# Performance work log

Hardware: AMD Instinct MI355X
Metric: run time of the kernel (lower is better)

The kernel has to match this reference:

```python
import jax, jax.numpy as jnp
import numpy as np

B, N, D = 4, 256, 256
H, DH = 4, 64
INNER = H * DH
L, MULT, EDGE, KNN = 2, 2, 11, 3
LN_EPS = 1e-5


def _layernorm(x, w, b):
    m = x.mean(-1, keepdims=True)
    v = ((x - m) ** 2).mean(-1, keepdims=True)
    return (x - m) * jax.lax.rsqrt(v + LN_EPS) * w + b


def _gelu(x):
    return jax.nn.gelu(x, approximate=False)  # torch nn.GELU default = exact erf


def _knn_pair_mask(coords, valid, k):
    # coords [B,M,2], valid [B,M] -> symmetric KNN adjacency among neighbors
    Bm, M = valid.shape
    d = jnp.sqrt(jnp.sum((coords[:, :, None, :] - coords[:, None, :, :]) ** 2, -1))
    eye = jnp.eye(M, dtype=bool)[None]
    inv = ~(valid[:, :, None] & valid[:, None, :])
    d = jnp.where(inv | eye, jnp.inf, d)
    neg, idx = jax.lax.top_k(-d, k)  # k smallest distances
    finite = jnp.isfinite(neg)
    bi = jnp.arange(Bm)[:, None, None]
    ri = jnp.arange(M)[None, :, None]
    mask = jnp.zeros((Bm, M, M), bool).at[bi, ri, idx].set(finite)
    mask = mask | jnp.swapaxes(mask, 1, 2)
    return mask & ~eye


def _build_graph(x, coords):
    # valid node mask (infer_valid_node_mask) and hop ids (infer_hop_ids)
    valid = (jnp.abs(x).sum(-1) > 0).at[:, 0].set(True)
    hop = jnp.ones((B, N), jnp.int32).at[:, 0].set(0)
    hop = hop.at[:, 1 + (N - 1) // 2:].set(2)
    eye = jnp.eye(N, dtype=bool)[None]
    adj = jnp.broadcast_to(eye, (B, N, N))
    nv = valid[:, 1:]
    adj = adj.at[:, 0, 1:].set(nv)
    adj = adj.at[:, 1:, 0].set(nv)
    npm = _knn_pair_mask(coords[:, 1:], nv, min(KNN, N - 2))
    adj = adj.at[:, 1:, 1:].set(adj[:, 1:, 1:] | npm)
    vp = valid[:, :, None] & valid[:, None, :]
    adj = adj & (vp | eye)
    # edge features [B,N,N,11]
    rel = coords[:, None, :, :] - coords[:, :, None, :]  # coords[j]-coords[i]
    dx, dy = rel[..., 0], rel[..., 1]
    dist = jnp.sqrt(dx ** 2 + dy ** 2 + 1e-8)
    cdist = jnp.sqrt(coords[..., 0] ** 2 + coords[..., 1] ** 2 + 1e-8)
    nvm = valid.at[:, 0].set(False)
    cd = jnp.where(nvm, cdist, 0.0)
    cnt = jnp.clip(nvm.sum(-1), 1).astype(x.dtype)
    ls = cd.sum(-1) / cnt
    ls = jnp.where(ls > 0, ls, 1.0)
    ndist = dist / jnp.clip(ls, 1e-6)[:, None, None]
    idx = jnp.arange(N)
    ones2 = jnp.ones((N, N), bool)
    qic = (idx[:, None] == 0) & ones2
    kic = (idx[None, :] == 0) & ones2
    eye2 = jnp.eye(N, dtype=bool)
    isnn = ~(qic | kic | eye2)
    same_hop = hop[:, :, None] == hop[:, None, :]
    hop_delta = jnp.abs(hop[:, None, :] - hop[:, :, None]).astype(x.dtype)
    same_ct = jnp.zeros((B, N, N), x.dtype)  # cell_inf is None
    f = lambda m: jnp.broadcast_to(m.astype(x.dtype), (B, N, N))
    edge_attr = jnp.stack(
        [dx, dy, dist, ndist, f(qic), f(kic), f(eye2), f(isnn),
         same_hop.astype(x.dtype), hop_delta, same_ct], -1)
    return adj, edge_attr


def _forward(x, coords, Wq, Wk, Wv, eb_w1, eb_b1, eb_w2, eb_b2,
             ev_w1, ev_b1, ev_w2, ev_b2, Wo, bo,
             ln1_w, ln1_b, ln2_w, ln2_b, ff_w1, ff_b1, ff_w2, ff_b2):
    adj, e = _build_graph(x, coords)
    scale = DH ** -0.5
    big = jnp.finfo(x.dtype).max
    for l in range(L):
        xn = _layernorm(x, ln1_w[l], ln1_b[l])
        q = (xn @ Wq[l]).reshape(B, N, H, DH).transpose(0, 2, 1, 3)  # b h n d
        k = (xn @ Wk[l]).reshape(B, N, H, DH).transpose(0, 2, 1, 3)
        v = (xn @ Wv[l]).reshape(B, N, H, DH).transpose(0, 2, 1, 3)
        eb = _gelu(e @ eb_w1[l] + eb_b1[l]) @ eb_w2[l] + eb_b2[l]  # [B,N,N,H]
        ev = _gelu(e @ ev_w1[l] + ev_b1[l]) @ ev_w2[l] + ev_b2[l]  # [B,N,N,INNER]
        ev = ev.reshape(B, N, N, H, DH).transpose(0, 3, 1, 2, 4)   # b h i j d
        sim = jnp.einsum('bhid,bhjd->bhij', q, k) * scale + eb.transpose(0, 3, 1, 2)
        sim = jnp.where(adj[:, None], sim, -big)
        attn = jax.nn.softmax(sim, -1)
        msgs = v[:, :, None, :, :] + ev                            # value injection
        out = jnp.einsum('bhij,bhijd->bhid', attn, msgs)
        out = out.transpose(0, 2, 1, 3).reshape(B, N, INNER) @ Wo[l] + bo[l]
        x = x + out
        xn2 = _layernorm(x, ln2_w[l], ln2_b[l])
        hg = xn2 @ ff_w1[l] + ff_b1[l]
        a, g = jnp.split(hg, 2, -1)  # GEGLU
        x = x + ((a * _gelu(g)) @ ff_w2[l] + ff_b2[l])
    return x


def setup_inputs() -> dict:
    key = jax.random.key(0)
    ks = iter(jax.random.split(key, 32))
    w = lambda shape, s=0.05: jax.random.normal(next(ks), shape, jnp.float32) * s
    return {
        'x': jax.random.normal(next(ks), (B, N, D), jnp.float32),
        'coords': jax.random.normal(next(ks), (B, N, 2), jnp.float32) * 3.0,
        'Wq': w((L, D, INNER)), 'Wk': w((L, D, INNER)), 'Wv': w((L, D, INNER)),
        'eb_w1': w((L, EDGE, INNER)), 'eb_b1': jnp.zeros((L, INNER)),
        'eb_w2': w((L, INNER, H)), 'eb_b2': jnp.zeros((L, H)),
        'ev_w1': w((L, EDGE, INNER)), 'ev_b1': jnp.zeros((L, INNER)),
        'ev_w2': w((L, INNER, INNER)), 'ev_b2': jnp.zeros((L, INNER)),
        'Wo': w((L, INNER, D)), 'bo': jnp.zeros((L, D)),
        'ln1_w': jnp.ones((L, D)), 'ln1_b': jnp.zeros((L, D)),
        'ln2_w': jnp.ones((L, D)), 'ln2_b': jnp.zeros((L, D)),
        'ff_w1': w((L, D, 2 * MULT * D)), 'ff_b1': jnp.zeros((L, 2 * MULT * D)),
        'ff_w2': w((L, MULT * D, D)), 'ff_b2': jnp.zeros((L, D)),
    }


def reference(x, coords, Wq, Wk, Wv, eb_w1, eb_b1, eb_w2, eb_b2,
              ev_w1, ev_b1, ev_w2, ev_b2, Wo, bo,
              ln1_w, ln1_b, ln2_w, ln2_b, ff_w1, ff_b1, ff_w2, ff_b2):
    return _forward(x, coords, Wq, Wk, Wv, eb_w1, eb_b1, eb_w2, eb_b2,
                    ev_w1, ev_b1, ev_w2, ev_b2, Wo, bo,
                    ln1_w, ln1_b, ln2_w, ln2_b, ff_w1, ff_b1, ff_w2, ff_b2)
```

## Files before the change

### kernel.cpp

```cpp
#include <hip/hip_runtime.h>


#define MAXE  16384
#define NONX  22080
#define BF16_TOTAL 1441792

typedef __attribute__((ext_vector_type(8))) short bf16x8;
typedef __attribute__((ext_vector_type(4))) float f32x4;

struct PtrPack { const void* p[23]; };

__device__ __forceinline__ float bf2f(unsigned short s) {
  return __uint_as_float(((unsigned)s) << 16);
}
__device__ __forceinline__ unsigned short f2bf(float f) {
  unsigned u = __float_as_uint(f);
  u += 0x7fffu + ((u >> 16) & 1u);
  return (unsigned short)(u >> 16);
}
__device__ __forceinline__ float gelu_f(float x) {
  return 0.5f * x * (1.0f + erff(x * 0.70710678118654752440f));
}
__device__ __forceinline__ float wave_red_sum(float v) {
#pragma unroll
  for (int o = 32; o > 0; o >>= 1) v += __shfl_xor(v, o);
  return v;
}

__device__ __forceinline__ void edge_feats(int i, int j, float cxi, float cyi,
                                           float cxj, float cyj, float lsd, float* e) {
  float dx = cxj - cxi, dy = cyj - cyi;
  float dist = sqrtf(dx * dx + dy * dy + 1e-8f);
  e[0] = dx; e[1] = dy; e[2] = dist; e[3] = dist / lsd;
  bool qic = (i == 0), kic = (j == 0), eye = (i == j);
  e[4] = qic ? 1.f : 0.f;
  e[5] = kic ? 1.f : 0.f;
  e[6] = eye ? 1.f : 0.f;
  e[7] = (!qic && !kic && !eye) ? 1.f : 0.f;
  int hi = (i == 0) ? 0 : ((i < 128) ? 1 : 2);
  int hj = (j == 0) ? 0 : ((j < 128) ? 1 : 2);
  e[8] = (hi == hj) ? 1.f : 0.f;
  int hd = hj - hi;
  e[9] = (float)(hd < 0 ? -hd : hd);
}

__global__ __launch_bounds__(256) void k_convert(PtrPack pp, float* __restrict__ blobF,
                                                 unsigned short* __restrict__ blobB,
                                                 int* __restrict__ valid,
                                                 float* __restrict__ rowsum,
                                                 int* __restrict__ gctr) {
  bool isf32 = (*(const unsigned*)pp.p[15] == 0x3F800000u);
  int t = threadIdx.x;
  if (blockIdx.x == 0 && t == 0) *gctr = 0;
  if (blockIdx.x < 1024) {
    if (blockIdx.x < 32) rowsum[blockIdx.x * 256 + t] = 0.f;
    int r = blockIdx.x;
    int idx = r * 256 + t;
    float v = isf32 ? ((const float*)pp.p[0])[idx]
                    : bf2f(((const unsigned short*)pp.p[0])[idx]);
    blobF[idx] = v;
    __shared__ float s[4];
    float a = wave_red_sum(fabsf(v));
    if ((t & 63) == 0) s[t >> 6] = a;
    __syncthreads();
    if (t == 0) valid[r] = ((s[0] + s[1] + s[2] + s[3]) > 0.0f) || ((r & 255) == 0);
  } else {
    const int fst[16] = {0,2048,7680,8192,10240,10304,15936,16448,16960,17472,17984,18496,19008,19520,21568,22080};
    const int fsz[15] = {2048,5632,512,2048,8,5632,512,512,512,512,512,512,512,2048,512};
    const int fin[15] = {1,5,6,7,8,9,10,12,14,15,16,17,18,20,22};
    const int bst[8]  = {0,131072,262144,393216,524288,655360,1179648,1441792};
    const int bin[7]  = {2,3,4,13,11,19,21};
    for (int idx = (blockIdx.x - 1024) * 256 + t; idx < NONX + BF16_TOTAL; idx += 1024 * 256) {
      if (idx < NONX) {
        int s = 0;
        while (s < 14 && idx >= fst[s + 1]) ++s;
        int e = idx - fst[s];
        float v = 0.f;
        if (e < fsz[s]) v = isf32 ? ((const float*)pp.p[fin[s]])[e]
                                  : bf2f(((const unsigned short*)pp.p[fin[s]])[e]);
        blobF[262144 + idx] = v;
      } else {
        int bi = idx - NONX;
        int s = 0;
        while (s < 6 && bi >= bst[s + 1]) ++s;
        int e = bi - bst[s];
        blobB[bi] = isf32 ? f2bf(((const float*)pp.p[bin[s]])[e])
                          : ((const unsigned short*)pp.p[bin[s]])[e];
      }
    }
  }
}

__global__ __launch_bounds__(256) void k_knn(const float* __restrict__ cf,
                                             const int* __restrict__ valid,
                                             int* __restrict__ knn) {
  int blk = blockIdx.x;
  int b = blk >> 6;
  int w = threadIdx.x >> 6, lane = threadIdx.x & 63;
  int i = (blk & 63) * 4 + w;
  const float2* cc = (const float2*)(cf + b * 512);
  float2 ci = cc[i];
  bool vi = (valid[b * 256 + i] != 0) && (i != 0);
  unsigned long long key[4];
#pragma unroll
  for (int k = 0; k < 4; ++k) {
    int j = lane + 64 * k;
    bool ok = vi && (j != 0) && (j != i) && (valid[b * 256 + j] != 0);
    unsigned long long kk = ~0ull;
    if (ok) {
      float2 cj = cc[j];
      float dx = ci.x - cj.x, dy = ci.y - cj.y;
      float dd = sqrtf(dx * dx + dy * dy);
      kk = (((unsigned long long)__float_as_uint(dd)) << 32) | (unsigned)j;
    }
    key[k] = kk;
  }
  int out[3];
#pragma unroll
  for (int rnd = 0; rnd < 3; ++rnd) {
    unsigned long long m = key[0];
    if (key[1] < m) m = key[1];
    if (key[2] < m) m = key[2];
    if (key[3] < m) m = key[3];
#pragma unroll
    for (int o = 32; o > 0; o >>= 1) {
      unsigned long long om = __shfl_xor(m, o);
      if (om < m) m = om;
    }
    out[rnd] = (m != ~0ull) ? (int)(m & 0xFFFFFFFFull) : -1;
#pragma unroll
    for (int k = 0; k < 4; ++k)
      if (key[k] == m) key[k] = ~0ull;
  }
  if (lane == 0) {
    knn[(b * 256 + i) * 3 + 0] = out[0];
    knn[(b * 256 + i) * 3 + 1] = out[1];
    knn[(b * 256 + i) * 3 + 2] = out[2];
  }
}

__global__ __launch_bounds__(256) void k_csr(const float* __restrict__ cf,
                                             const int* __restrict__ valid,
                                             const int* __restrict__ knn,
                                             float* __restrict__ lsbuf,
                                             int* __restrict__ deg, int* __restrict__ rowptr,
                                             int* __restrict__ rowof, int* __restrict__ colsb,
                                             int* __restrict__ gctr) {
  int b = blockIdx.x, t = threadIdx.x;
  __shared__ unsigned adjw[256][8];
  __shared__ float sred[8];
  __shared__ int wsum[4];
  __shared__ int sbase;

  int r = b * 256 + t;
  float cx = cf[r * 2 + 0], cy = cf[r * 2 + 1];
  int lv = valid[r];
#pragma unroll
  for (int w = 0; w < 8; ++w) adjw[t][w] = 0u;
  __syncthreads();

  atomicOr(&adjw[t][t >> 5], 1u << (t & 31));
  if (t >= 1 && lv) {
    atomicOr(&adjw[0][t >> 5], 1u << (t & 31));
    atomicOr(&adjw[t][0], 1u);
  }
#pragma unroll
  for (int s = 0; s < 3; ++s) {
    int j = knn[r * 3 + s];
    if (j >= 0) {
      atomicOr(&adjw[t][j >> 5], 1u << (j & 31));
      atomicOr(&adjw[j][t >> 5], 1u << (t & 31));
    }
  }
  float cdist = sqrtf(cx * cx + cy * cy + 1e-8f);
  int nvm = (t >= 1) && lv;
  float rs = wave_red_sum(nvm ? cdist : 0.0f);
  float rc = wave_red_sum(nvm ? 1.0f : 0.0f);
  if ((t & 63) == 0) { sred[t >> 6] = rs; sred[4 + (t >> 6)] = rc; }
  __syncthreads();

  if (t == 0) {
    float totd = sred[0] + sred[1] + sred[2] + sred[3];
    float totc = sred[4] + sred[5] + sred[6] + sred[7];
    float ls = totd / fmaxf(totc, 1.0f);
    ls = (ls > 0.0f) ? ls : 1.0f;
    lsbuf[b] = fmaxf(ls, 1e-6f);
  }

  int dg = 0;
#pragma unroll
  for (int w = 0; w < 8; ++w) dg += __popc(adjw[t][w]);

  int lane = t & 63, wv = t >> 6;
  int x = dg;
#pragma unroll
  for (int off = 1; off < 64; off <<= 1) {
    int y = __shfl_up(x, off);
    if (lane >= off) x += y;
  }
  if (lane == 63) wsum[wv] = x;
  __syncthreads();
  if (t == 0) sbase = atomicAdd(gctr, wsum[0] + wsum[1] + wsum[2] + wsum[3]);
  __syncthreads();
  int woff = 0;
#pragma unroll
  for (int k2 = 0; k2 < 4; ++k2) woff += (k2 < wv) ? wsum[k2] : 0;
  int off0 = sbase + woff + x - dg;

  rowptr[r] = off0;
  deg[r] = dg;
  int o = off0;
#pragma unroll
  for (int w = 0; w < 8; ++w) {
    unsigned bits = adjw[t][w];
    while (bits) {
      int bp = __ffs(bits) - 1;
      colsb[o] = w * 32 + bp;
      rowof[o] = r;
      ++o;
      bits &= bits - 1;
    }
  }
}

template <int AMODE, int OMODE>
__device__ __forceinline__ void mfma_body(const void* Aptr, int lda,
                                          const unsigned short* __restrict__ B, int ldb, int n0B,
                                          const float* __restrict__ bias,
                                          const float* resid,
                                          void* C, int ldc, int n0C,
                                          int m0, int K, bool obf,
                                          const float* __restrict__ lnG,
                                          const float* __restrict__ lnB) {
  __shared__ short As[16][72];
  __shared__ short Bs[64][72];
  __shared__ float sG[256], sB2[256], sMean[16], sRstd[16];
  int t = threadIdx.x, lane = t & 63, w = t >> 6;

  if (AMODE == 3) {
    sG[t] = lnG[t]; sB2[t] = lnB[t];
    int row = t >> 4, sub = t & 15;
    const float* xr = (const float*)Aptr + (size_t)(m0 + row) * lda + sub * 16;
    float s = 0.f, ss = 0.f;
#pragma unroll
    for (int ii = 0; ii < 4; ++ii) {
      float4 v4 = *(const float4*)(xr + ii * 4);
      s += v4.x + v4.y + v4.z + v4.w;
      ss += v4.x * v4.x + v4.y * v4.y + v4.z * v4.z + v4.w * v4.w;
    }
    s += __shfl_xor(s, 1); s += __shfl_xor(s, 2);
    s += __shfl_xor(s, 4); s += __shfl_xor(s, 8);
    ss += __shfl_xor(ss, 1); ss += __shfl_xor(ss, 2);
    ss += __shfl_xor(ss, 4); ss += __shfl_xor(ss, 8);
    if (sub == 0) {
      float m = s * (1.f / 256.f);
      float var = ss * (1.f / 256.f) - m * m;
      sMean[row] = m;
      sRstd[row] = 1.f / sqrtf(var + 1e-5f);
    }
    __syncthreads();
  }

  f32x4 acc;
  acc[0] = 0.f; acc[1] = 0.f; acc[2] = 0.f; acc[3] = 0.f;

  int am = t >> 3, ak = (t & 7) * 8;
  int bk = t >> 2, bn = (t & 3) * 16;

  for (int k0 = 0; k0 < K; k0 += 64) {
    if (t < 128) {
      if (AMODE == 0) {
        const unsigned short* ap = (const unsigned short*)Aptr + (size_t)(m0 + am) * lda + k0 + ak;
        *(bf16x8*)&As[am][ak] = *(const bf16x8*)ap;
      } else if (AMODE == 1) {
        const float* ap = (const float*)Aptr + (size_t)(m0 + am) * lda + k0 + ak;
        float4 a0 = *(const float4*)ap;
        float4 a1 = *(const float4*)(ap + 4);
        float4 g0 = *(const float4*)(ap + 512);
        float4 g1 = *(const float4*)(ap + 516);
        short tmp[8];
        tmp[0] = (short)f2bf(a0.x * gelu_f(g0.x));
        tmp[1] = (short)f2bf(a0.y * gelu_f(g0.y));
        tmp[2] = (short)f2bf(a0.z * gelu_f(g0.z));
        tmp[3] = (short)f2bf(a0.w * gelu_f(g0.w));
        tmp[4] = (short)f2bf(a1.x * gelu_f(g1.x));
        tmp[5] = (short)f2bf(a1.y * gelu_f(g1.y));
        tmp[6] = (short)f2bf(a1.z * gelu_f(g1.z));
        tmp[7] = (short)f2bf(a1.w * gelu_f(g1.w));
        *(bf16x8*)&As[am][ak] = *(bf16x8*)tmp;
      } else if (AMODE == 2) {
        const float* ap = (const float*)Aptr + (size_t)(m0 + am) * lda + k0 + ak;
        float4 a0 = *(const float4*)ap;
        float4 a1 = *(const float4*)(ap + 4);
        short tmp[8];
        tmp[0] = (short)f2bf(a0.x); tmp[1] = (short)f2bf(a0.y);
        tmp[2] = (short)f2bf(a0.z); tmp[3] = (short)f2bf(a0.w);
        tmp[4] = (short)f2bf(a1.x); tmp[5] = (short)f2bf(a1.y);
        tmp[6] = (short)f2bf(a1.z); tmp[7] = (short)f2bf(a1.w);
        *(bf16x8*)&As[am][ak] = *(bf16x8*)tmp;
      } else {
        const float* ap = (const float*)Aptr + (size_t)(m0 + am) * lda + k0 + ak;
        float4 a0 = *(const float4*)ap;
        float4 a1 = *(const float4*)(ap + 4);
        float mm = sMean[am], rr = sRstd[am];
        short tmp[8];
        int kb = k0 + ak;
        tmp[0] = (short)f2bf((a0.x - mm) * rr * sG[kb + 0] + sB2[kb + 0]);
        tmp[1] = (short)f2bf((a0.y - mm) * rr * sG[kb + 1] + sB2[kb + 1]);
        tmp[2] = (short)f2bf((a0.z - mm) * rr * sG[kb + 2] + sB2[kb + 2]);
        tmp[3] = (short)f2bf((a0.w - mm) * rr * sG[kb + 3] + sB2[kb + 3]);
        tmp[4] = (short)f2bf((a1.x - mm) * rr * sG[kb + 4] + sB2[kb + 4]);
        tmp[5] = (short)f2bf((a1.y - mm) * rr * sG[kb + 5] + sB2[kb + 5]);
        tmp[6] = (short)f2bf((a1.z - mm) * rr * sG[kb + 6] + sB2[kb + 6]);
        tmp[7] = (short)f2bf((a1.w - mm) * rr * sG[kb + 7] + sB2[kb + 7]);
        *(bf16x8*)&As[am][ak] = *(bf16x8*)tmp;
      }
    }
    {
      const unsigned short* bp = B + (size_t)(k0 + bk) * ldb + n0B + bn;
      bf16x8 bv0 = *(const bf16x8*)bp;
      bf16x8 bv1 = *(const bf16x8*)(bp + 8);
#pragma unroll
      for (int i2 = 0; i2 < 8; ++i2) Bs[bn + i2][bk] = bv0[i2];
#pragma unroll
      for (int i2 = 0; i2 < 8; ++i2) Bs[bn + 8 + i2][bk] = bv1[i2];
    }
    __syncthreads();
    int q = lane >> 4;
    bf16x8 af0 = *(const bf16x8*)&As[lane & 15][q * 8];
    bf16x8 af1 = *(const bf16x8*)&As[lane & 15][32 + q * 8];
    bf16x8 bf0 = *(const bf16x8*)&Bs[w * 16 + (lane & 15)][q * 8];
    bf16x8 bf1 = *(const bf16x8*)&Bs[w * 16 + (lane & 15)][32 + q * 8];
    acc = __builtin_amdgcn_mfma_f32_16x16x32_bf16(af0, bf0, acc, 0, 0, 0);
    acc = __builtin_amdgcn_mfma_f32_16x16x32_bf16(af1, bf1, acc, 0, 0, 0);
    __syncthreads();
  }

  int q = lane >> 4;
  int cn = w * 16 + (lane & 15);
  int col = n0C + cn;
  float bv = bias ? bias[n0B + cn] : 0.0f;
#pragma unroll
  for (int rr = 0; rr < 4; ++rr) {
    int row = m0 + q * 4 + rr;
    float v = acc[rr] + bv;
    if (resid) v += resid[(size_t)row * ldc + col];
    if (OMODE == 2 || (OMODE == 1 && obf)) {
      ((unsigned short*)C)[(size_t)row * ldc + col] = f2bf(v);
    } else {
      ((float*)C)[(size_t)row * ldc + col] = v;
    }
  }
}

template <int AMODE, int OMODE>
__global__ __launch_bounds__(256) void k_mfma(const void* A, int lda, int aYoffBytes,
                                              const unsigned short* B, int ldb,
                                              const float* bias, const float* resid,
                                              void* C, int ldc, int K,
                                              const unsigned* probe,
                                              const float* lnG, const float* lnB) {
  bool obf = (OMODE == 1) && probe && (*probe != 0x3F800000u);
  int n0 = blockIdx.y * 64;
  const void* Ap = (const char*)A + (size_t)aYoffBytes * blockIdx.y;
  mfma_body<AMODE, OMODE>(Ap, lda, B, ldb, n0, bias, resid, C, ldc, n0,
                          blockIdx.x * 16, K, obf, lnG, lnB);
}

__global__ __launch_bounds__(256) void k_mfma_qkv(const float* X,
                                                  const float* lnG, const float* lnB,
                                                  const unsigned short* WqL, float* qkv) {
  int sel = blockIdx.y >> 2;
  const unsigned short* B = WqL + sel * 131072;
  int n0B = (blockIdx.y & 3) * 64;
  int n0C = blockIdx.y * 64;
  mfma_body<3, 0>(X, 256, B, 256, n0B, nullptr, nullptr, qkv, 768, n0C,
                  blockIdx.x * 16, 256, false, lnG, lnB);
}

__global__ __launch_bounds__(256) void k_simz(const float* __restrict__ cf,
                                              const float* __restrict__ qkv,
                                              const int* __restrict__ rowof,
                                              const int* __restrict__ colsb,
                                              const int* __restrict__ gctr,
                                              const float* __restrict__ lsbuf,
                                              const float* __restrict__ ebW1,
                                              const float* __restrict__ ebB1,
                                              const float* __restrict__ ebW2,
                                              const float* __restrict__ ebB2,
                                              float* __restrict__ esim,
                                              float* __restrict__ rowsum,
                                              float* __restrict__ tb,
                                              float* __restrict__ vs) {
  int t = threadIdx.x;
  {
    size_t tz = (size_t)blockIdx.x * 1024 + t;
    tb[tz] = 0.f; tb[tz + 256] = 0.f; tb[tz + 512] = 0.f; tb[tz + 768] = 0.f;
    vs[(size_t)blockIdx.x * 256 + t] = 0.f;
  }
  int E = *gctr;
  int lane = t & 63, w = t >> 6;
  float W1r[4][10], B1r[4], W2r[4][4];
#pragma unroll
  for (int kk = 0; kk < 4; ++kk) {
    int c = kk * 64 + lane;
    B1r[kk] = ebB1[c];
#pragma unroll
    for (int f = 0; f < 10; ++f) W1r[kk][f] = ebW1[f * 256 + c];
    float4 w2 = *(const float4*)(ebW2 + c * 4);
    W2r[kk][0] = w2.x; W2r[kk][1] = w2.y; W2r[kk][2] = w2.z; W2r[kk][3] = w2.w;
  }
  float b20 = ebB2[0], b21 = ebB2[1], b22 = ebB2[2], b23 = ebB2[3];
  for (int g = blockIdx.x * 4 + w; g < E; g += 4096) {
    int r = rowof[g], j = colsb[g];
    int b = r >> 8, i = r & 255;
    float ls = lsbuf[b];
    const float2* cc = (const float2*)cf;
    float2 ci = cc[b * 256 + i], cj = cc[b * 256 + j];
    float ef[10];
    edge_feats(i, j, ci.x, ci.y, cj.x, cj.y, ls, ef);
    float red[8];
#pragma unroll
    for (int z = 0; z < 8; ++z) red[z] = 0.0f;
#pragma unroll
    for (int kk = 0; kk < 4; ++kk) {
      int c = kk * 64 + lane;
      float h1 = B1r[kk];
#pragma unroll
      for (int f = 0; f < 10; ++f) h1 += ef[f] * W1r[kk][f];
      float g1 = gelu_f(h1);
      red[4] += g1 * W2r[kk][0];
      red[5] += g1 * W2r[kk][1];
      red[6] += g1 * W2r[kk][2];
      red[7] += g1 * W2r[kk][3];
      red[kk] = qkv[(size_t)r * 768 + c] * qkv[((size_t)(b * 256 + j)) * 768 + 256 + c];
    }
#pragma unroll
    for (int z = 0; z < 8; ++z) {
#pragma unroll
      for (int o = 32; o > 0; o >>= 1) red[z] += __shfl_xor(red[z], o);
    }
    if (lane == 0) {
      float e0 = expf(red[0] * 0.125f + red[4] + b20);
      float e1 = expf(red[1] * 0.125f + red[5] + b21);
      float e2 = expf(red[2] * 0.125f + red[6] + b22);
      float e3 = expf(red[3] * 0.125f + red[7] + b23);
      *(float4*)&esim[(size_t)g * 4] = make_float4(e0, e1, e2, e3);
      atomicAdd(&rowsum[r * 4 + 0], e0);
      atomicAdd(&rowsum[r * 4 + 1], e1);
      atomicAdd(&rowsum[r * 4 + 2], e2);
      atomicAdd(&rowsum[r * 4 + 3], e3);
    }
  }
}

__global__ __launch_bounds__(256, 4) void k_accum(const float* __restrict__ cf,
                                                  const float* __restrict__ qkv,
                                                  const int* __restrict__ rowptr,
                                                  const int* __restrict__ deg,
                                                  const int* __restrict__ colsb,
                                                  const float* __restrict__ esim,
                                                  const float* __restrict__ rowsum,
                                                  const float* __restrict__ lsbuf,
                                                  const float* __restrict__ evW1,
                                                  const float* __restrict__ evB1,
                                                  float* __restrict__ tb,
                                                  float* __restrict__ vs) {
  int x = blockIdx.x;
  int r, ch;
  if (x < 1024) { r = x; ch = 0; }
  else { int i5 = x - 1024; r = (i5 / 7) * 256; ch = 1 + i5 % 7; }
  int d = deg[r];
  int e0 = ch * 32;
  if (e0 >= d) return;
  int n = min(32, d - e0);
  int base = rowptr[r] + e0;
  int b = r >> 8, i = r & 255;
  int u = threadIdx.x, h = u >> 6;

  __shared__ int scols[32];
  __shared__ float4 sattn[32];
  __shared__ float sef[32][10];
  if (u < n) {
    float4 S4 = *(const float4*)&rowsum[r * 4];
    int j = colsb[base + u];
    scols[u] = j;
    float4 e = *(const float4*)&esim[(size_t)(base + u) * 4];
    sattn[u] = make_float4(e.x / S4.x, e.y / S4.y, e.z / S4.z, e.w / S4.w);
    float ls = lsbuf[b];
    const float2* cc = (const float2*)cf;
    float2 ci = cc[b * 256 + i], cj = cc[b * 256 + j];
    float ef[10];
    edge_feats(i, j, ci.x, ci.y, cj.x, cj.y, ls, ef);
#pragma unroll
    for (int f = 0; f < 10; ++f) sef[u][f] = ef[f];
  }
  __syncthreads();

  float evb = evB1[u];
  float w1r[10];
#pragma unroll
  for (int f = 0; f < 10; ++f) w1r[f] = evW1[f * 256 + u];
  float t0 = 0.f, t1 = 0.f, t2 = 0.f, t3 = 0.f, va = 0.f;
#pragma unroll 4
  for (int e = 0; e < n; ++e) {
    float4 a = sattn[e];
    int j = scols[e];
    float h1 = evb;
#pragma unroll
    for (int f = 0; f < 10; ++f) h1 += sef[e][f] * w1r[f];
    float g1 = gelu_f(h1);
    t0 += a.x * g1; t1 += a.y * g1; t2 += a.z * g1; t3 += a.w * g1;
    float ah = (h == 0) ? a.x : (h == 1) ? a.y : (h == 2) ? a.z : a.w;
    va += ah * qkv[((size_t)(b * 256 + j)) * 768 + 512 + u];
  }
  size_t tbase = (size_t)r * 1024 + u;
  atomicAdd(&tb[tbase], t0);
  atomicAdd(&tb[tbase + 256], t1);
  atomicAdd(&tb[tbase + 512], t2);
  atomicAdd(&tb[tbase + 768], t3);
  atomicAdd(&vs[(size_t)r * 256 + u], va);
}

extern "C" void kernel_launch(void* const* d_in, const int* in_sizes, int n_in,
                              void* d_out, int out_size, void* d_ws, size_t ws_size,
                              hipStream_t stream) {
  (void)in_sizes; (void)n_in; (void)out_size; (void)ws_size;

  char* wp = (char*)d_ws;
  auto carve = [&](size_t bytes) -> char* {
    char* p = wp;
    wp += ((bytes + 255) / 256) * 256;
    return p;
  };
  int*   gctr   = (int*)carve(4);
  float* lsb    = (float*)carve(16);
  int*   valid  = (int*)carve(1024 * 4);
  int*   deg    = (int*)carve(1024 * 4);
  int*   rowptr = (int*)carve(1024 * 4);
  int*   rowof  = (int*)carve(MAXE * 4);
  int*   colsb  = (int*)carve(MAXE * 4);
  int*   knn    = (int*)carve(1024 * 3 * 4);
  float* rowsum = (float*)carve(8192 * 4);
  float* sim    = (float*)carve((size_t)MAXE * 16);
  float* blobF  = (float*)carve((size_t)(262144 + NONX) * 4);
  unsigned short* blobB = (unsigned short*)carve((size_t)BF16_TOTAL * 2);
  float* qkv    = (float*)carve((size_t)1024 * 768 * 4);
  float* xcur   = (float*)carve((size_t)262144 * 4);
  float* tb     = (float*)carve((size_t)1048576 * 4);
  float* vs     = (float*)carve((size_t)262144 * 4);
  unsigned short* oi = (unsigned short*)carve((size_t)262144 * 2);

  const float* Xf    = blobF + 0;
  const float* Cf    = blobF + 262144;
  const float* ebW1  = blobF + 264192;
  const float* ebB1  = blobF + 269824;
  const float* ebW2  = blobF + 270336;
  const float* ebB2  = blobF + 272384;
  const float* evW1  = blobF + 272448;
  const float* evB1  = blobF + 278080;
  const float* evB2  = blobF + 278592;
  const float* boB   = blobF + 279104;
  const float* ln1w  = blobF + 279616;
  const float* ln1b  = blobF + 280128;
  const float* ln2w  = blobF + 280640;
  const float* ln2b  = blobF + 281152;
  const float* ffb1  = blobF + 281664;
  const float* ffb2  = blobF + 283712;
  const unsigned short* WqB   = blobB + 0;
  const unsigned short* WoB   = blobB + 393216;
  const unsigned short* evW2B = blobB + 524288;
  const unsigned short* ffw1B = blobB + 655360;
  const unsigned short* ffw2B = blobB + 1179648;

  PtrPack pp;
  for (int i = 0; i < 23; ++i) pp.p[i] = d_in[i];
  const unsigned* probe = (const unsigned*)d_in[15];

  k_convert<<<2048, 256, 0, stream>>>(pp, blobF, blobB, valid, rowsum, gctr);
  k_knn<<<256, 256, 0, stream>>>(Cf, valid, knn);
  k_csr<<<4, 256, 0, stream>>>(Cf, valid, knn, lsb, deg, rowptr, rowof, colsb, gctr);

  for (int l = 0; l < 2; ++l) {
    const float* xsrc = (l == 0) ? Xf : xcur;
    float* rsumL = rowsum + l * 4096;
    k_mfma_qkv<<<dim3(64, 12), 256, 0, stream>>>(xsrc, ln1w + l * 256, ln1b + l * 256,
                                                 WqB + l * 65536, qkv);
    k_simz<<<1024, 256, 0, stream>>>(Cf, qkv, rowof, colsb, gctr, lsb,
                                     ebW1 + l * 2816, ebB1 + l * 256,
                                     ebW2 + l * 1024, ebB2 + l * 4,
                                     sim, rsumL, tb, vs);
    k_accum<<<1052, 256, 0, stream>>>(Cf, qkv, rowptr, deg, colsb, sim, rsumL, lsb,
                                      evW1 + l * 2816, evB1 + l * 256, tb, vs);
    k_mfma<2, 2><<<dim3(64, 4), 256, 0, stream>>>(tb, 1024, 1024, evW2B + l * 65536, 256,
                                                  evB2 + l * 256, vs, oi, 256, 256,
                                                  nullptr, nullptr, nullptr);
    k_mfma<0, 0><<<dim3(64, 4), 256, 0, stream>>>(oi, 256, 0, WoB + l * 65536, 256,
                                                  boB + l * 256, xsrc, xcur, 256, 256,
                                                  nullptr, nullptr, nullptr);
    k_mfma<3, 0><<<dim3(64, 16), 256, 0, stream>>>(xcur, 256, 0, ffw1B + l * 262144, 1024,
                                                   ffb1 + l * 1024, nullptr, tb, 1024, 256,
                                                   nullptr, ln2w + l * 256, ln2b + l * 256);
    if (l == 0) {
      k_mfma<1, 0><<<dim3(64, 4), 256, 0, stream>>>(tb, 1024, 0, ffw2B + l * 131072, 256,
                                                    ffb2 + l * 256, xcur, xcur, 256, 512,
                                                    nullptr, nullptr, nullptr);
    } else {
      k_mfma<1, 1><<<dim3(64, 4), 256, 0, stream>>>(tb, 1024, 0, ffw2B + l * 131072, 256,
                                                    ffb2 + l * 256, xcur, d_out, 256, 512,
                                                    probe, nullptr, nullptr);
    }
  }
}
```

Before: 306.8 us.

## Batch global loads per 256-wide K chunk in GEMM and vectorize bf16 weight packing

```diff
diff --git a/kernel.cpp b/kernel.cpp
--- a/kernel.cpp
+++ b/kernel.cpp
@@ -70,22 +70,29 @@
     const int fin[15] = {1,5,6,7,8,9,10,12,14,15,16,17,18,20,22};
     const int bst[8]  = {0,131072,262144,393216,524288,655360,1179648,1441792};
     const int bin[7]  = {2,3,4,13,11,19,21};
-    for (int idx = (blockIdx.x - 1024) * 256 + t; idx < NONX + BF16_TOTAL; idx += 1024 * 256) {
-      if (idx < NONX) {
+    const int NUNITS = NONX + BF16_TOTAL / 4;
+    for (int u = (blockIdx.x - 1024) * 256 + t; u < NUNITS; u += 1024 * 256) {
+      if (u < NONX) {
         int s = 0;
-        while (s < 14 && idx >= fst[s + 1]) ++s;
-        int e = idx - fst[s];
+        while (s < 14 && u >= fst[s + 1]) ++s;
+        int e = u - fst[s];
         float v = 0.f;
         if (e < fsz[s]) v = isf32 ? ((const float*)pp.p[fin[s]])[e]
                                   : bf2f(((const unsigned short*)pp.p[fin[s]])[e]);
-        blobF[262144 + idx] = v;
+        blobF[262144 + u] = v;
       } else {
-        int bi = idx - NONX;
+        int bi = (u - NONX) * 4;
         int s = 0;
         while (s < 6 && bi >= bst[s + 1]) ++s;
         int e = bi - bst[s];
-        blobB[bi] = isf32 ? f2bf(((const float*)pp.p[bin[s]])[e])
-                          : ((const unsigned short*)pp.p[bin[s]])[e];
+        ushort4 o;
+        if (isf32) {
+          const float* sp = (const float*)pp.p[bin[s]] + e;
+          o.x = f2bf(sp[0]); o.y = f2bf(sp[1]); o.z = f2bf(sp[2]); o.w = f2bf(sp[3]);
+        } else {
+          o = *(const ushort4*)((const unsigned short*)pp.p[bin[s]] + e);
+        }
+        *(ushort4*)&blobB[bi] = o;
       }
     }
   }
@@ -234,106 +241,122 @@
                                           const float* __restrict__ lnB) {
   __shared__ short As[16][72];
   __shared__ short Bs[64][72];
-  __shared__ float sG[256], sB2[256], sMean[16], sRstd[16];
+  __shared__ float sG[256], sB2[256];
   int t = threadIdx.x, lane = t & 63, w = t >> 6;
 
-  if (AMODE == 3) {
-    sG[t] = lnG[t]; sB2[t] = lnB[t];
-    int row = t >> 4, sub = t & 15;
-    const float* xr = (const float*)Aptr + (size_t)(m0 + row) * lda + sub * 16;
-    float s = 0.f, ss = 0.f;
-#pragma unroll
-    for (int ii = 0; ii < 4; ++ii) {
-      float4 v4 = *(const float4*)(xr + ii * 4);
-      s += v4.x + v4.y + v4.z + v4.w;
-      ss += v4.x * v4.x + v4.y * v4.y + v4.z * v4.z + v4.w * v4.w;
-    }
-    s += __shfl_xor(s, 1); s += __shfl_xor(s, 2);
-    s += __shfl_xor(s, 4); s += __shfl_xor(s, 8);
-    ss += __shfl_xor(ss, 1); ss += __shfl_xor(ss, 2);
-    ss += __shfl_xor(ss, 4); ss += __shfl_xor(ss, 8);
-    if (sub == 0) {
-      float m = s * (1.f / 256.f);
-      float var = ss * (1.f / 256.f) - m * m;
-      sMean[row] = m;
-      sRstd[row] = 1.f / sqrtf(var + 1e-5f);
-    }
-    __syncthreads();
-  }
+  int am = t >> 3, ak = (t & 7) * 8;
+  int bk = t >> 2, bn = (t & 3) * 16;
 
   f32x4 acc;
   acc[0] = 0.f; acc[1] = 0.f; acc[2] = 0.f; acc[3] = 0.f;
 
-  int am = t >> 3, ak = (t & 7) * 8;
-  int bk = t >> 2, bn = (t & 3) * 16;
-
-  for (int k0 = 0; k0 < K; k0 += 64) {
-    if (t < 128) {
-      if (AMODE == 0) {
-        const unsigned short* ap = (const unsigned short*)Aptr + (size_t)(m0 + am) * lda + k0 + ak;
-        *(bf16x8*)&As[am][ak] = *(const bf16x8*)ap;
-      } else if (AMODE == 1) {
-        const float* ap = (const float*)Aptr + (size_t)(m0 + am) * lda + k0 + ak;
-        float4 a0 = *(const float4*)ap;
-        float4 a1 = *(const float4*)(ap + 4);
-        float4 g0 = *(const float4*)(ap + 512);
-        float4 g1 = *(const float4*)(ap + 516);
-        short tmp[8];
-        tmp[0] = (short)f2bf(a0.x * gelu_f(g0.x));
-        tmp[1] = (short)f2bf(a0.y * gelu_f(g0.y));
-        tmp[2] = (short)f2bf(a0.z * gelu_f(g0.z));
-        tmp[3] = (short)f2bf(a0.w * gelu_f(g0.w));
-        tmp[4] = (short)f2bf(a1.x * gelu_f(g1.x));
-        tmp[5] = (short)f2bf(a1.y * gelu_f(g1.y));
-        tmp[6] = (short)f2bf(a1.z * gelu_f(g1.z));
-        tmp[7] = (short)f2bf(a1.w * gelu_f(g1.w));
-        *(bf16x8*)&As[am][ak] = *(bf16x8*)tmp;
-      } else if (AMODE == 2) {
-        const float* ap = (const float*)Aptr + (size_t)(m0 + am) * lda + k0 + ak;
-        float4 a0 = *(const float4*)ap;
-        float4 a1 = *(const float4*)(ap + 4);
-        short tmp[8];
-        tmp[0] = (short)f2bf(a0.x); tmp[1] = (short)f2bf(a0.y);
-        tmp[2] = (short)f2bf(a0.z); tmp[3] = (short)f2bf(a0.w);
-        tmp[4] = (short)f2bf(a1.x); tmp[5] = (short)f2bf(a1.y);
-        tmp[6] = (short)f2bf(a1.z); tmp[7] = (short)f2bf(a1.w);
-        *(bf16x8*)&As[am][ak] = *(bf16x8*)tmp;
-      } else {
-        const float* ap = (const float*)Aptr + (size_t)(m0 + am) * lda + k0 + ak;
-        float4 a0 = *(const float4*)ap;
-        float4 a1 = *(const float4*)(ap + 4);
-        float mm = sMean[am], rr = sRstd[am];
-        short tmp[8];
-        int kb = k0 + ak;
-        tmp[0] = (short)f2bf((a0.x - mm) * rr * sG[kb + 0] + sB2[kb + 0]);
-        tmp[1] = (short)f2bf((a0.y - mm) * rr * sG[kb + 1] + sB2[kb + 1]);
-        tmp[2] = (short)f2bf((a0.z - mm) * rr * sG[kb + 2] + sB2[kb + 2]);
-        tmp[3] = (short)f2bf((a0.w - mm) * rr * sG[kb + 3] + sB2[kb + 3]);
-        tmp[4] = (short)f2bf((a1.x - mm) * rr * sG[kb + 4] + sB2[kb + 4]);
-        tmp[5] = (short)f2bf((a1.y - mm) * rr * sG[kb + 5] + sB2[kb + 5]);
-        tmp[6] = (short)f2bf((a1.z - mm) * rr * sG[kb + 6] + sB2[kb + 6]);
-        tmp[7] = (short)f2bf((a1.w - mm) * rr * sG[kb + 7] + sB2[kb + 7]);
-        *(bf16x8*)&As[am][ak] = *(bf16x8*)tmp;
+  for (int kc = 0; kc < K; kc += 256) {
+    bf16x8 aB[4];
+    float4 aF[4][2];
+    float4 gF[4][2];
+    bf16x8 bR[4][2];
+#pragma unroll
+    for (int r = 0; r < 4; ++r) {
+      int k0 = kc + r * 64;
+      if (t < 128) {
+        if (AMODE == 0) {
+          aB[r] = *(const bf16x8*)((const unsigned short*)Aptr +
+                                   (size_t)(m0 + am) * lda + k0 + ak);
+        } else {
+          const float* ap = (const float*)Aptr + (size_t)(m0 + am) * lda + k0 + ak;
+          aF[r][0] = *(const float4*)ap;
+          aF[r][1] = *(const float4*)(ap + 4);
+          if (AMODE == 1) {
+            gF[r][0] = *(const float4*)(ap + 512);
+            gF[r][1] = *(const float4*)(ap + 516);
+          }
+        }
       }
-    }
-    {
       const unsigned short* bp = B + (size_t)(k0 + bk) * ldb + n0B + bn;
-      bf16x8 bv0 = *(const bf16x8*)bp;
-      bf16x8 bv1 = *(const bf16x8*)(bp + 8);
-#pragma unroll
-      for (int i2 = 0; i2 < 8; ++i2) Bs[bn + i2][bk] = bv0[i2];
-#pragma unroll
-      for (int i2 = 0; i2 < 8; ++i2) Bs[bn + 8 + i2][bk] = bv1[i2];
-    }
-    __syncthreads();
-    int q = lane >> 4;
-    bf16x8 af0 = *(const bf16x8*)&As[lane & 15][q * 8];
-    bf16x8 af1 = *(const bf16x8*)&As[lane & 15][32 + q * 8];
-    bf16x8 bf0 = *(const bf16x8*)&Bs[w * 16 + (lane & 15)][q * 8];
-    bf16x8 bf1 = *(const bf16x8*)&Bs[w * 16 + (lane & 15)][32 + q * 8];
-    acc = __builtin_amdgcn_mfma_f32_16x16x32_bf16(af0, bf0, acc, 0, 0, 0);
-    acc = __builtin_amdgcn_mfma_f32_16x16x32_bf16(af1, bf1, acc, 0, 0, 0);
-    __syncthreads();
+      bR[r][0] = *(const bf16x8*)bp;
+      bR[r][1] = *(const bf16x8*)(bp + 8);
+    }
+
+    float mm = 0.f, rstd = 0.f;
+    if (AMODE == 3) {
+      sG[t] = lnG[t]; sB2[t] = lnB[t];
+      if (t < 128) {
+        float s = 0.f, ss = 0.f;
+#pragma unroll
+        for (int r = 0; r < 4; ++r)
+#pragma unroll
+          for (int h2 = 0; h2 < 2; ++h2) {
+            float4 v4 = aF[r][h2];
+            s += v4.x + v4.y + v4.z + v4.w;
+            ss += v4.x * v4.x + v4.y * v4.y + v4.z * v4.z + v4.w * v4.w;
+          }
+        s += __shfl_xor(s, 1); s += __shfl_xor(s, 2); s += __shfl_xor(s, 4);
+        ss += __shfl_xor(ss, 1); ss += __shfl_xor(ss, 2); ss += __shfl_xor(ss, 4);
+        mm = s * (1.f / 256.f);
+        float var = ss * (1.f / 256.f) - mm * mm;
+        rstd = 1.f / sqrtf(var + 1e-5f);
+      }
+      __syncthreads();
+    }
+
+#pragma unroll
+    for (int r = 0; r < 4; ++r) {
+      if (t < 128) {
+        if (AMODE == 0) {
+          *(bf16x8*)&As[am][ak] = aB[r];
+        } else if (AMODE == 1) {
+          float4 a0 = aF[r][0], a1 = aF[r][1];
+          float4 g0 = gF[r][0], g1 = gF[r][1];
+          short tmp[8];
+          tmp[0] = (short)f2bf(a0.x * gelu_f(g0.x));
+          tmp[1] = (short)f2bf(a0.y * gelu_f(g0.y));
+          tmp[2] = (short)f2bf(a0.z * gelu_f(g0.z));
+          tmp[3] = (short)f2bf(a0.w * gelu_f(g0.w));
+          tmp[4] = (short)f2bf(a1.x * gelu_f(g1.x));
+          tmp[5] = (short)f2bf(a1.y * gelu_f(g1.y));
+          tmp[6] = (short)f2bf(a1.z * gelu_f(g1.z));
+          tmp[7] = (short)f2bf(a1.w * gelu_f(g1.w));
+          *(bf16x8*)&As[am][ak] = *(bf16x8*)tmp;
+        } else if (AMODE == 2) {
+          float4 a0 = aF[r][0], a1 = aF[r][1];
+          short tmp[8];
+          tmp[0] = (short)f2bf(a0.x); tmp[1] = (short)f2bf(a0.y);
+          tmp[2] = (short)f2bf(a0.z); tmp[3] = (short)f2bf(a0.w);
+          tmp[4] = (short)f2bf(a1.x); tmp[5] = (short)f2bf(a1.y);
+          tmp[6] = (short)f2bf(a1.z); tmp[7] = (short)f2bf(a1.w);
+          *(bf16x8*)&As[am][ak] = *(bf16x8*)tmp;
+        } else {
+          float4 a0 = aF[r][0], a1 = aF[r][1];
+          int kb = kc + r * 64 + ak;
+          short tmp[8];
+          tmp[0] = (short)f2bf((a0.x - mm) * rstd * sG[kb + 0] + sB2[kb + 0]);
+          tmp[1] = (short)f2bf((a0.y - mm) * rstd * sG[kb + 1] + sB2[kb + 1]);
+          tmp[2] = (short)f2bf((a0.z - mm) * rstd * sG[kb + 2] + sB2[kb + 2]);
+          tmp[3] = (short)f2bf((a0.w - mm) * rstd * sG[kb + 3] + sB2[kb + 3]);
+          tmp[4] = (short)f2bf((a1.x - mm) * rstd * sG[kb + 4] + sB2[kb + 4]);
+          tmp[5] = (short)f2bf((a1.y - mm) * rstd * sG[kb + 5] + sB2[kb + 5]);
+          tmp[6] = (short)f2bf((a1.z - mm) * rstd * sG[kb + 6] + sB2[kb + 6]);
+          tmp[7] = (short)f2bf((a1.w - mm) * rstd * sG[kb + 7] + sB2[kb + 7]);
+          *(bf16x8*)&As[am][ak] = *(bf16x8*)tmp;
+        }
+      }
+      {
+        bf16x8 bv0 = bR[r][0], bv1 = bR[r][1];
+#pragma unroll
+        for (int i2 = 0; i2 < 8; ++i2) Bs[bn + i2][bk] = bv0[i2];
+#pragma unroll
+        for (int i2 = 0; i2 < 8; ++i2) Bs[bn + 8 + i2][bk] = bv1[i2];
+      }
+      __syncthreads();
+      int q = lane >> 4;
+      bf16x8 af0 = *(const bf16x8*)&As[lane & 15][q * 8];
+      bf16x8 af1 = *(const bf16x8*)&As[lane & 15][32 + q * 8];
+      bf16x8 bf0 = *(const bf16x8*)&Bs[w * 16 + (lane & 15)][q * 8];
+      bf16x8 bf1 = *(const bf16x8*)&Bs[w * 16 + (lane & 15)][32 + q * 8];
+      acc = __builtin_amdgcn_mfma_f32_16x16x32_bf16(af0, bf0, acc, 0, 0, 0);
+      acc = __builtin_amdgcn_mfma_f32_16x16x32_bf16(af1, bf1, acc, 0, 0, 0);
+      __syncthreads();
+    }
   }
 
   int q = lane >> 4;
```

After: 289.7 us. -5.6%, faster.
